# Optimization experiments

Measured on AMD Instinct MI355X. Metric: run time of the kernel, lower is better.

The kernel has to match this reference:

```python
import jax, jax.numpy as jnp
import numpy as np
import math

EPS = 1e-5

def _bn_lrelu(x, g, b, m, v):
    # BatchNorm2d (eval, running stats) + LeakyReLU(0.01)
    inv = jax.lax.rsqrt(v + EPS)
    xn = (x - m[None, :, None, None]) * (g * inv)[None, :, None, None] + b[None, :, None, None]
    return jnp.where(xn >= 0, xn, 0.01 * xn)

def _conv3x3(x, w, b):
    # zero pad 1 on freq (dim2) and time (dim3) (pad_left state is None -> zeros), valid 3x3 conv
    x = jnp.pad(x, ((0, 0), (0, 0), (1, 1), (1, 1)))
    y = jax.lax.conv_general_dilated(x, w, (1, 1), 'VALID',
                                     dimension_numbers=('NCHW', 'OIHW', 'NCHW'))
    return y + b[None, :, None, None]

def _conv1x1(x, w, b):
    return jnp.einsum('bcft,oc->boft', x, w[:, :, 0, 0]) + b[None, :, None, None]

def _blockx3(x, g, b, m, v, w, wb):
    return _conv3x3(_bn_lrelu(x, g, b, m, v), w, wb)

def _mha(x, wqkv, bqkv, wo, bo, n_heads=4, L=64, U=128):
    # banded local attention over time, window = (L back, L fwd), chunked by U
    B, C, F, T = x.shape
    H = n_heads; D = C // H; S = 2 * L
    qkv = _conv1x1(x, wqkv, bqkv)                 # [B,3C,F,T]
    qkv = qkv.transpose(0, 2, 1, 3)               # [B,F,3C,T]
    def split(a):
        return a.reshape(B * F, H, D, T).transpose(0, 1, 3, 2)  # [BF,H,T,D]
    q = split(qkv[:, :, :C])
    k = split(qkv[:, :, C:2 * C])
    v = split(qkv[:, :, 2 * C:])
    Tkv = T + L                                   # kv padded left by L (zero state)
    nC = T // U
    pad_to = nC * U + S                           # pad kv right so every chunk window exists
    kp = jnp.pad(k, ((0, 0), (0, 0), (L, pad_to - Tkv), (0, 0)))
    vp = jnp.pad(v, ((0, 0), (0, 0), (L, pad_to - Tkv), (0, 0)))
    idx = (jnp.arange(nC) * U)[:, None] + jnp.arange(U + S)[None, :]   # [nC, U+S]
    kc = kp[:, :, idx, :]                         # [BF,H,nC,U+S,D]
    vc = vp[:, :, idx, :]
    qc = q.reshape(B * F, H, nC, U, D)
    i = jnp.arange(U)[:, None]; j = jnp.arange(U + S)[None, :]
    band = (j >= i) & (j <= i + S)                # row i sees cols i..i+S (width 1+2L)
    valid = (jnp.arange(nC)[:, None] * U + jnp.arange(U + S)[None, :]) < Tkv
    mask = (band[None, :, :] & valid[:, None, :]).astype(x.dtype)      # [nC,U,U+S]
    scores = jnp.einsum('bhcqd,bhckd->bhcqk', qc, kc) / math.sqrt(D)
    scores = scores * mask - 10000.0 * (1.0 - mask)
    p = jax.nn.softmax(scores, axis=-1)
    o = jnp.einsum('bhcqk,bhckd->bhcqd', p, vc)   # [BF,H,nC,U,D]
    o = o.reshape(B * F, H, T, D).transpose(0, 1, 3, 2).reshape(B, F, C, T).transpose(0, 2, 1, 3)
    return _conv1x1(o, wo, bo)

def setup_inputs() -> dict:
    key = jax.random.key(0)
    ks = jax.random.split(key, 40)
    d = {}
    d['x'] = jax.random.normal(ks[0], (4, 64, 64, 512), dtype=jnp.float32)
    def bn(i, c, pre):
        d[pre + '_g'] = jax.random.normal(ks[i], (c,), jnp.float32) * 0.1 + 1.0
        d[pre + '_b'] = jax.random.normal(ks[i + 1], (c,), jnp.float32) * 0.1
        d[pre + '_m'] = jax.random.normal(ks[i + 2], (c,), jnp.float32) * 0.1
        d[pre + '_v'] = jax.random.uniform(ks[i + 3], (c,), jnp.float32, 0.5, 1.5)
    def conv(i, o, c, kh, kw, pre):
        fan = c * kh * kw
        d[pre + '_w'] = jax.random.normal(ks[i], (o, c, kh, kw), jnp.float32) / math.sqrt(fan)
        d[pre + '_wb'] = jax.random.normal(ks[i + 1], (o,), jnp.float32) * 0.01
    bn(1, 64, 'bd0');  conv(5, 32, 64, 3, 3, 'bd0')
    bn(7, 96, 'bd1');  conv(11, 32, 96, 3, 3, 'bd1')
    bn(13, 128, 'bdo'); conv(17, 64, 128, 3, 3, 'bdo')
    d['qkv_w'] = jax.random.normal(ks[19], (192, 64, 1, 1), jnp.float32) / math.sqrt(64)
    d['qkv_b'] = jax.random.normal(ks[20], (192,), jnp.float32) * 0.01
    d['o_w'] = jax.random.normal(ks[21], (64, 64, 1, 1), jnp.float32) / math.sqrt(64)
    d['o_b'] = jax.random.normal(ks[22], (64,), jnp.float32) * 0.01
    bn(23, 128, 'sao'); conv(27, 64, 128, 1, 1, 'sao')
    return d

def reference(x,
              bd0_g, bd0_b, bd0_m, bd0_v, bd0_w, bd0_wb,
              bd1_g, bd1_b, bd1_m, bd1_v, bd1_w, bd1_wb,
              bdo_g, bdo_b, bdo_m, bdo_v, bdo_w, bdo_wb,
              qkv_w, qkv_b, o_w, o_b,
              sao_g, sao_b, sao_m, sao_v, sao_w, sao_wb):
    # dense conv stack: 64 -> +32 -> +32 -> 64
    a0 = _blockx3(x, bd0_g, bd0_b, bd0_m, bd0_v, bd0_w, bd0_wb)
    x1 = jnp.concatenate([x, a0], axis=1)                 # [B,96,F,T]
    a1 = _blockx3(x1, bd1_g, bd1_b, bd1_m, bd1_v, bd1_w, bd1_wb)
    x2 = jnp.concatenate([x1, a1], axis=1)                # [B,128,F,T]
    y = _blockx3(x2, bdo_g, bdo_b, bdo_m, bdo_v, bdo_w, bdo_wb)  # [B,64,F,T]
    # banded self-attention branch
    att = _mha(y, qkv_w, qkv_b, o_w, o_b)                 # [B,64,F,T]
    z = jnp.concatenate([y, att], axis=1)                 # [B,128,F,T]
    out = _conv1x1(_bn_lrelu(z, sao_g, sao_b, sao_m, sao_v), sao_w, sao_wb)
    return out
```

## Files before the change

### kernel.cpp

```cpp
#include <hip/hip_runtime.h>
#include <hip/hip_bf16.h>

typedef unsigned short u16t;
typedef __attribute__((ext_vector_type(8))) short bfrag;
typedef __attribute__((ext_vector_type(4))) float f32x4;
typedef __attribute__((ext_vector_type(8))) unsigned short uh8;

__device__ __forceinline__ float bfu(u16t u) {
    union { unsigned int i; float f; } c;
    c.i = ((unsigned int)u) << 16;
    return c.f;
}
__device__ __forceinline__ u16t fbf(float f) {
    __hip_bfloat16 h = __float2bfloat16(f);
    return *reinterpret_cast<u16t*>(&h);
}

__global__ __launch_bounds__(256) void prep_x_k(
    const float* __restrict__ x, u16t* __restrict__ xt)
{
    constexpr int F = 64, T = 512;
    __shared__ u16t su[64][74];
    const int tid = threadIdx.x;
    const int t0 = blockIdx.x * 64;
    const int f = blockIdx.y, b = blockIdx.z;

#pragma unroll
    for (int p = 0; p < 16; p++) {
        int i = tid + 256 * p;
        int c = i >> 6, t = i & 63;
        su[c][t] = fbf(x[(((long)b * 64 + c) * F + f) * T + t0 + t]);
    }
    __syncthreads();
#pragma unroll
    for (int p = 0; p < 2; p++) {
        int i = tid + 256 * p;
        int t = i >> 3, c8 = i & 7;
        uh8 v;
#pragma unroll
        for (int j = 0; j < 8; j++) v[j] = su[c8 * 8 + j][t];
        *(uh8*)&xt[(((long)b * F + f) * T + t0 + t) * 64 + c8 * 8] = v;
    }
}

__global__ __launch_bounds__(256) void prep_w_k(
    const float* __restrict__ w0, const float* __restrict__ w1,
    const float* __restrict__ w2, const float* __restrict__ ow,
    const float* __restrict__ sw, const float* __restrict__ qw,
    u16t* __restrict__ wp)
{
    int idx = blockIdx.x * 256 + threadIdx.x;
    if (idx >= 144384) return;
    if (idx < 119808) {
        int C_IN, C_OUT, e;
        const float* src;
        if (idx < 18432)      { C_IN = 64;  C_OUT = 32; src = w0; e = idx; }
        else if (idx < 46080) { C_IN = 96;  C_OUT = 32; src = w1; e = idx - 18432; }
        else                  { C_IN = 128; C_OUT = 64; src = w2; e = idx - 46080; }
        int NCOT = C_OUT / 16;
        int j  = e & 7;
        int l  = (e >> 3) & 63;
        int r  = e >> 9;
        int ct = r % NCOT;
        int r2 = r / NCOT;
        int kk = r2 % 9;
        int cb = r2 / 9;
        int co  = ct * 16 + (l & 15);
        int kin = cb * 32 + (l >> 4) * 8 + j;
        int kh = kk / 3, kw = kk % 3;
        wp[idx] = fbf(src[((co * C_IN + kin) * 3 + kh) * 3 + kw]);
    } else if (idx < 123904) {
        int e = idx - 119808;
        int ks = e & 31, co = (e >> 5) & 63, kb = e >> 11;
        wp[idx] = fbf(ow[co * 64 + kb * 32 + ks]);
    } else if (idx < 132096) {
        int e = idx - 123904;
        int ks = e & 31, co = (e >> 5) & 63, kb = e >> 11;
        wp[idx] = fbf(sw[co * 128 + kb * 32 + ks]);
    } else {
        int e = idx - 132096;
        int ks = e & 31, co = (e >> 5) % 192, kb = e / 6144;
        wp[idx] = fbf(qw[co * 64 + kb * 32 + ks]);
    }
}

template<int C_IN, int C_OUT, bool OBF>
__global__ __launch_bounds__(256) void conv3x3_mfma_k(
    const u16t* __restrict__ s0, const u16t* __restrict__ s1,
    const u16t* __restrict__ s2,
    const float* __restrict__ gg, const float* __restrict__ bb,
    const float* __restrict__ mm, const float* __restrict__ vv,
    const u16t* __restrict__ wseg, const float* __restrict__ wb,
    void* __restrict__ dstv)
{
    constexpr int F = 64, T = 512, TT = 64;
    constexpr int NCH  = C_IN / 32;
    constexpr int NCOT = C_OUT / 16;
    constexpr int WT   = 9 * NCOT * 64;

    __shared__ __align__(16) u16t s_x[3][66][40];
    __shared__ __align__(16) u16t s_w[WT * 8];
    __shared__ float s_scA[C_IN], s_shA[C_IN];

    const int tid = threadIdx.x;
    const int t0 = blockIdx.x * TT;
    const int f  = blockIdx.y;
    const int b  = blockIdx.z;

    if (tid < C_IN) {
        float s = gg[tid] * rsqrtf(vv[tid] + 1e-5f);
        s_scA[tid] = s;
        s_shA[tid] = bb[tid] - mm[tid] * s;
    }

    const int l  = tid & 63;
    const int wv = tid >> 6;
    const int lr = l & 15;
    const int lq = l >> 4;
    const int tbase = wv * 16 + lr;

    f32x4 acc[NCOT];
#pragma unroll
    for (int i = 0; i < NCOT; i++) acc[i] = (f32x4){0.f, 0.f, 0.f, 0.f};

    for (int ch = 0; ch < NCH; ch++) {
        __syncthreads();

        for (int idx = tid; idx < 792 + WT; idx += 256) {
            if (idx < 792) {
                int row = idx >> 2, oct = idx & 3;
                int kh = (row >= 132) ? 2 : ((row >= 66) ? 1 : 0);
                int tp = row - kh * 66;
                int fi = f + kh - 1;
                int tg = t0 + tp - 1;
                int gc8 = ch * 4 + oct;
                uh8 v = (uh8)0;
                if ((unsigned)fi < (unsigned)F && (unsigned)tg < (unsigned)T) {
                    const u16t* sp; int coff, cw;
                    if (gc8 < 8)       { sp = s0; coff = gc8 * 8;        cw = 64; }
                    else if (gc8 < 12) { sp = s1; coff = (gc8 - 8) * 8;  cw = 32; }
                    else               { sp = s2; coff = (gc8 - 12) * 8; cw = 32; }
                    uh8 raw = *(const uh8*)&sp[(((long)b * F + fi) * T + tg) * cw + coff];
#pragma unroll
                    for (int j = 0; j < 8; j++) {
                        float xv = bfu(raw[j]);
                        float xn = fmaf(xv, s_scA[gc8 * 8 + j], s_shA[gc8 * 8 + j]);
                        v[j] = fbf(fmaxf(xn, 0.01f * xn));
                    }
                }
                *(uh8*)&s_x[kh][tp][oct * 8] = v;
            } else {
                int w = idx - 792;
                *(uh8*)&s_w[w * 8] = *(const uh8*)&wseg[((long)ch * WT + w) * 8];
            }
        }
        __syncthreads();

#pragma unroll
        for (int kk = 0; kk < 9; kk++) {
            const int kh = kk / 3, kw = kk % 3;
            bfrag B = *(const bfrag*)&s_x[kh][tbase + kw][lq * 8];
#pragma unroll
            for (int ct = 0; ct < NCOT; ct++) {
                bfrag A = *(const bfrag*)&s_w[((kk * NCOT + ct) * 64 + l) * 8];
                acc[ct] = __builtin_amdgcn_mfma_f32_16x16x32_bf16(A, B, acc[ct], 0, 0, 0);
            }
        }
    }

    const int t = t0 + wv * 16 + lr;
#pragma unroll
    for (int ct = 0; ct < NCOT; ct++) {
        int co0 = ct * 16 + lq * 4;
        float4 bs = *(const float4*)&wb[co0];
        long obase = (((long)b * F + f) * T + t) * C_OUT + co0;
        if (OBF) {
            u16t* dp = (u16t*)dstv;
            ushort4 pk;
            pk.x = fbf(acc[ct][0] + bs.x);
            pk.y = fbf(acc[ct][1] + bs.y);
            pk.z = fbf(acc[ct][2] + bs.z);
            pk.w = fbf(acc[ct][3] + bs.w);
            *(ushort4*)&dp[obase] = pk;
        } else {
            float* dp = (float*)dstv;
            float4 ov;
            ov.x = acc[ct][0] + bs.x;
            ov.y = acc[ct][1] + bs.y;
            ov.z = acc[ct][2] + bs.z;
            ov.w = acc[ct][3] + bs.w;
            *(float4*)&dp[obase] = ov;
        }
    }
}

__global__ __launch_bounds__(256) void qkv_mfma_k(
    const u16t* __restrict__ ybf, const u16t* __restrict__ wq,
    const float* __restrict__ qbias,
    u16t* __restrict__ q_t, u16t* __restrict__ k_t, u16t* __restrict__ v_t)
{
    constexpr int F = 64, T = 512;
    __shared__ __align__(16) u16t s_y[64][72];
    const int tid = threadIdx.x;
    const int t0 = blockIdx.x * 64;
    const int f = blockIdx.y, b = blockIdx.z;
    const long bf = (long)b * F + f;

    for (int i = tid; i < 512; i += 256) {
        int tt = i >> 3, c0 = (i & 7) * 8;
        *(uh8*)&s_y[tt][c0] = *(const uh8*)&ybf[(bf * T + t0 + tt) * 64 + c0];
    }
    __syncthreads();

    const int l = tid & 63, wv = tid >> 6;
    const int lr = l & 15, lq = l >> 4;
    const int tb = wv * 16 + lr;

    bfrag B0 = *(const bfrag*)&s_y[tb][lq * 8];
    bfrag B1 = *(const bfrag*)&s_y[tb][32 + lq * 8];

    f32x4 acc[12];
#pragma unroll
    for (int i = 0; i < 12; i++) acc[i] = (f32x4){0.f, 0.f, 0.f, 0.f};
#pragma unroll
    for (int ct = 0; ct < 12; ct++) {
        bfrag A0 = *(const bfrag*)&wq[(ct * 16 + lr) * 32 + lq * 8];
        acc[ct] = __builtin_amdgcn_mfma_f32_16x16x32_bf16(A0, B0, acc[ct], 0, 0, 0);
    }
#pragma unroll
    for (int ct = 0; ct < 12; ct++) {
        bfrag A1 = *(const bfrag*)&wq[(192 + ct * 16 + lr) * 32 + lq * 8];
        acc[ct] = __builtin_amdgcn_mfma_f32_16x16x32_bf16(A1, B1, acc[ct], 0, 0, 0);
    }

    const int t = t0 + tb;
#pragma unroll
    for (int ct = 0; ct < 12; ct++) {
        int co0 = ct * 16 + lq * 4;
        float4 bi = *(const float4*)&qbias[co0];
        float a0 = acc[ct][0] + bi.x, a1 = acc[ct][1] + bi.y;
        float a2 = acc[ct][2] + bi.z, a3 = acc[ct][3] + bi.w;
        if (co0 < 64) {
            ushort4 pk;
            pk.x = fbf(a0 * 0.25f); pk.y = fbf(a1 * 0.25f);
            pk.z = fbf(a2 * 0.25f); pk.w = fbf(a3 * 0.25f);
            *(ushort4*)&q_t[(bf * T + t) * 64 + co0] = pk;
        } else if (co0 < 128) {
            int hh = (co0 - 64) >> 4, d0 = (co0 - 64) & 15;
            ushort4 pk;
            pk.x = fbf(a0); pk.y = fbf(a1); pk.z = fbf(a2); pk.w = fbf(a3);
            *(ushort4*)&k_t[((bf * 4 + hh) * T + t) * 16 + d0] = pk;
        } else {
            int hh = (co0 - 128) >> 4, d0 = (co0 - 128) & 15;
            long vb = (bf * 4 + hh) * 16;
            v_t[(vb + d0 + 0) * T + t] = fbf(a0);
            v_t[(vb + d0 + 1) * T + t] = fbf(a1);
            v_t[(vb + d0 + 2) * T + t] = fbf(a2);
            v_t[(vb + d0 + 3) * T + t] = fbf(a3);
        }
    }
}

__global__ __launch_bounds__(256) void attn_mfma_k(
    const u16t* __restrict__ qt, const u16t* __restrict__ kt_,
    const u16t* __restrict__ vt, u16t* __restrict__ ob)
{
    constexpr int T = 512, F = 64;
    const int qc = blockIdx.x & 7;
    const int h  = blockIdx.x >> 3;
    const int f = blockIdx.y, b = blockIdx.z;
    const int qb0 = qc * 64;
    const int tid = threadIdx.x;
    const long bf = (long)b * F + f;
    const long kvb = bf * 4 + h;

    __shared__ __align__(16) u16t s_k[192][24];
    __shared__ __align__(16) u16t s_v[16][216];
    __shared__ __align__(16) u16t s_p[4][16][168];
    __shared__ __align__(16) u16t s_zero[8];

    if (tid < 8) s_zero[tid] = 0;

    for (int idx = tid; idx < 384; idx += 256) {
        int kk = idx >> 1, hv = idx & 1;
        int p = qb0 - 64 + kk;
        uh8 v = (uh8)0;
        if ((unsigned)p < (unsigned)T)
            v = *(const uh8*)&kt_[(kvb * T + p) * 16 + hv * 8];
        *(uh8*)&s_k[kk][hv * 8] = v;
    }
    for (int idx = tid; idx < 432; idx += 256) {
        int d = idx / 27, c8 = idx % 27;
        int kk0 = c8 * 8;
        int p0 = qb0 - 64 + kk0;
        uh8 v = (uh8)0;
        if (p0 >= 0 && p0 + 7 < T) {
            v = *(const uh8*)&vt[(kvb * 16 + d) * T + p0];
        } else {
#pragma unroll
            for (int j = 0; j < 8; j++) {
                int p = p0 + j;
                v[j] = ((unsigned)p < (unsigned)T)
                     ? vt[(kvb * 16 + d) * T + p] : (u16t)0;
            }
        }
        *(uh8*)&s_v[d][kk0] = v;
    }
    __syncthreads();

    const int l  = tid & 63;
    const int wv = tid >> 6;
    const int lr = l & 15;
    const int lq = l >> 4;
    const int qt0 = qb0 + wv * 16;

    bfrag Bq = (bfrag)0;
    if (lq < 2)
        Bq = *(const bfrag*)&qt[(bf * T + qt0 + lr) * 64 + h * 16 + lq * 8];

    f32x4 sf[9];
#pragma unroll
    for (int kti = 0; kti < 9; kti++) {
        const u16t* ap = (lq < 2) ? &s_k[wv * 16 + kti * 16 + lr][lq * 8]
                                  : &s_zero[0];
        bfrag A = *(const bfrag*)ap;
        sf[kti] = __builtin_amdgcn_mfma_f32_16x16x32_bf16(
            A, Bq, (f32x4){0.f, 0.f, 0.f, 0.f}, 0, 0, 0);
    }

    float m = -3.0e38f;
#pragma unroll
    for (int kti = 0; kti < 9; kti++) {
#pragma unroll
        for (int j = 0; j < 4; j++) {
            int rk = kti * 16 + lq * 4 + j;
            int dq = rk - lr;
            int p  = qt0 - 64 + rk;
            float s = sf[kti][j];
            s = (dq >= 0 && dq <= 128 && p < T) ? s : -1.0e30f;
            sf[kti][j] = s;
            m = fmaxf(m, s);
        }
    }
    m = fmaxf(m, __shfl_xor(m, 16));
    m = fmaxf(m, __shfl_xor(m, 32));

    float lsum = 0.f;
#pragma unroll
    for (int kti = 0; kti < 9; kti++) {
#pragma unroll
        for (int j = 0; j < 4; j++) {
            float e = __expf(sf[kti][j] - m);
            sf[kti][j] = e;
            lsum += e;
        }
    }
    lsum += __shfl_xor(lsum, 16);
    lsum += __shfl_xor(lsum, 32);

#pragma unroll
    for (int kti = 0; kti < 9; kti++) {
        ushort4 pk;
        pk.x = fbf(sf[kti][0]); pk.y = fbf(sf[kti][1]);
        pk.z = fbf(sf[kti][2]); pk.w = fbf(sf[kti][3]);
        *(ushort4*)&s_p[wv][lr][kti * 16 + lq * 4] = pk;
    }
    {
        ushort4 z; z.x = 0; z.y = 0; z.z = 0; z.w = 0;
        *(ushort4*)&s_p[wv][lr][144 + lq * 4] = z;
    }
    __syncthreads();

    f32x4 oa = (f32x4){0.f, 0.f, 0.f, 0.f};
#pragma unroll
    for (int kc = 0; kc < 5; kc++) {
        bfrag Av = *(const bfrag*)&s_v[lr][wv * 16 + kc * 32 + lq * 8];
        bfrag Bp = *(const bfrag*)&s_p[wv][lr][kc * 32 + lq * 8];
        oa = __builtin_amdgcn_mfma_f32_16x16x32_bf16(Av, Bp, oa, 0, 0, 0);
    }
    const float inv = 1.0f / lsum;
    ushort4 ov;
    ov.x = fbf(oa[0] * inv); ov.y = fbf(oa[1] * inv);
    ov.z = fbf(oa[2] * inv); ov.w = fbf(oa[3] * inv);
    *(ushort4*)&ob[(bf * T + qt0 + lr) * 64 + h * 16 + lq * 4] = ov;
}

__global__ __launch_bounds__(256) void final_mfma_k(
    const u16t* __restrict__ ob, const u16t* __restrict__ yb,
    const u16t* __restrict__ wo, const float* __restrict__ obias,
    const float* __restrict__ sg, const float* __restrict__ sb,
    const float* __restrict__ sm, const float* __restrict__ sv,
    const u16t* __restrict__ wsao, const float* __restrict__ swb,
    float* __restrict__ out)
{
    constexpr int F = 64, T = 512, TT = 64, P = 72;
    __shared__ __align__(16) u16t s_ob[64][P];
    __shared__ __align__(16) u16t s_y2[64][P];
    __shared__ __align__(16) u16t s_att[64][P];
    __shared__ float s_sc[128], s_sh[128];

    const int tid = threadIdx.x;
    const int t0 = blockIdx.x * TT;
    const int f = blockIdx.y, b = blockIdx.z;

    if (tid < 128) {
        float sc = sg[tid] * rsqrtf(sv[tid] + 1e-5f);
        s_sc[tid] = sc;
        s_sh[tid] = sb[tid] - sm[tid] * sc;
    }
    __syncthreads();

    for (int i = tid; i < 512; i += 256) {
        int tt = i >> 3, c0 = (i & 7) * 8;
        long gi = (((long)b * F + f) * T + t0 + tt) * 64 + c0;
        *(uh8*)&s_ob[tt][c0] = *(const uh8*)&ob[gi];
        uh8 raw = *(const uh8*)&yb[gi];
        uh8 v;
#pragma unroll
        for (int j = 0; j < 8; j++) {
            float xv = bfu(raw[j]);
            float xn = fmaf(xv, s_sc[c0 + j], s_sh[c0 + j]);
            v[j] = fbf(fmaxf(xn, 0.01f * xn));
        }
        *(uh8*)&s_y2[tt][c0] = v;
    }
    __syncthreads();

    const int l  = tid & 63;
    const int wv = tid >> 6;
    const int lr = l & 15;
    const int lq = l >> 4;
    const int tbase = wv * 16 + lr;
    const int cbase = lq * 8;

    f32x4 acc1[4];
#pragma unroll
    for (int i = 0; i < 4; i++) acc1[i] = (f32x4){0.f, 0.f, 0.f, 0.f};
#pragma unroll
    for (int kb = 0; kb < 2; kb++) {
        bfrag B = *(const bfrag*)&s_ob[tbase][kb * 32 + cbase];
#pragma unroll
        for (int ct = 0; ct < 4; ct++) {
            bfrag A = *(const bfrag*)&wo[(kb * 64 + ct * 16 + lr) * 32 + lq * 8];
            acc1[ct] = __builtin_amdgcn_mfma_f32_16x16x32_bf16(A, B, acc1[ct], 0, 0, 0);
        }
    }
#pragma unroll
    for (int ct = 0; ct < 4; ct++) {
        int co = ct * 16 + lq * 4;
        float4 bi = *(const float4*)&obias[co];
#pragma unroll
        for (int j = 0; j < 4; j++) {
            float a = acc1[ct][j] + ((j == 0) ? bi.x : (j == 1) ? bi.y : (j == 2) ? bi.z : bi.w);
            int cg = 64 + co + j;
            float xn = fmaf(a, s_sc[cg], s_sh[cg]);
            s_att[tbase][co + j] = fbf(fmaxf(xn, 0.01f * xn));
        }
    }
    __syncthreads();

    f32x4 acc2[4];
#pragma unroll
    for (int i = 0; i < 4; i++) acc2[i] = (f32x4){0.f, 0.f, 0.f, 0.f};
#pragma unroll
    for (int kb = 0; kb < 4; kb++) {
        bfrag B = (kb < 2) ? *(const bfrag*)&s_y2[tbase][kb * 32 + cbase]
                           : *(const bfrag*)&s_att[tbase][(kb - 2) * 32 + cbase];
#pragma unroll
        for (int ct = 0; ct < 4; ct++) {
            bfrag A = *(const bfrag*)&wsao[(kb * 64 + ct * 16 + lr) * 32 + lq * 8];
            acc2[ct] = __builtin_amdgcn_mfma_f32_16x16x32_bf16(A, B, acc2[ct], 0, 0, 0);
        }
    }
    const int t = t0 + wv * 16 + lr;
#pragma unroll
    for (int ct = 0; ct < 4; ct++) {
        int co0 = ct * 16 + lq * 4;
        float4 bs = *(const float4*)&swb[co0];
#pragma unroll
        for (int j = 0; j < 4; j++) {
            float bv = (j == 0) ? bs.x : (j == 1) ? bs.y : (j == 2) ? bs.z : bs.w;
            out[(((long)b * 64 + co0 + j) * F + f) * T + t] = acc2[ct][j] + bv;
        }
    }
}

extern "C" void kernel_launch(void* const* d_in, const int* in_sizes, int n_in,
                              void* d_out, int out_size, void* d_ws, size_t ws_size,
                              hipStream_t stream)
{
    (void)in_sizes; (void)n_in; (void)out_size; (void)ws_size;

    const float* x      = (const float*)d_in[0];
    const float* bd0_g  = (const float*)d_in[1];
    const float* bd0_b  = (const float*)d_in[2];
    const float* bd0_m  = (const float*)d_in[3];
    const float* bd0_v  = (const float*)d_in[4];
    const float* bd0_w  = (const float*)d_in[5];
    const float* bd0_wb = (const float*)d_in[6];
    const float* bd1_g  = (const float*)d_in[7];
    const float* bd1_b  = (const float*)d_in[8];
    const float* bd1_m  = (const float*)d_in[9];
    const float* bd1_v  = (const float*)d_in[10];
    const float* bd1_w  = (const float*)d_in[11];
    const float* bd1_wb = (const float*)d_in[12];
    const float* bdo_g  = (const float*)d_in[13];
    const float* bdo_b  = (const float*)d_in[14];
    const float* bdo_m  = (const float*)d_in[15];
    const float* bdo_v  = (const float*)d_in[16];
    const float* bdo_w  = (const float*)d_in[17];
    const float* bdo_wb = (const float*)d_in[18];
    const float* qkv_w  = (const float*)d_in[19];
    const float* qkv_b  = (const float*)d_in[20];
    const float* o_w    = (const float*)d_in[21];
    const float* o_b    = (const float*)d_in[22];
    const float* sao_g  = (const float*)d_in[23];
    const float* sao_b  = (const float*)d_in[24];
    const float* sao_m  = (const float*)d_in[25];
    const float* sao_v  = (const float*)d_in[26];
    const float* sao_w  = (const float*)d_in[27];
    const float* sao_wb = (const float*)d_in[28];

    char* ws = (char*)d_ws;
    u16t* xt  = (u16t*)(ws);
    u16t* a0  = (u16t*)(ws + 16777216);
    u16t* a1  = (u16t*)(ws + 25165824);
    u16t* q_t = (u16t*)(ws);
    u16t* k_t = (u16t*)(ws + 16777216);
    u16t* v_t = (u16t*)(ws + 33554432);
    u16t* ybf = (u16t*)(ws + 50331648);
    u16t* obf = q_t;
    u16t* wpk = (u16t*)(ws + 67108864);

    dim3 blk(256);
    dim3 gconv(8, 64, 4);

    hipLaunchKernelGGL(prep_x_k, gconv, blk, 0, stream, x, xt);
    hipLaunchKernelGGL(prep_w_k, dim3(564), blk, 0, stream,
        bd0_w, bd1_w, bdo_w, o_w, sao_w, qkv_w, wpk);
    hipLaunchKernelGGL((conv3x3_mfma_k<64, 32, true>), gconv, blk, 0, stream,
        xt, nullptr, nullptr, bd0_g, bd0_b, bd0_m, bd0_v, wpk, bd0_wb, (void*)a0);
    hipLaunchKernelGGL((conv3x3_mfma_k<96, 32, true>), gconv, blk, 0, stream,
        xt, a0, nullptr, bd1_g, bd1_b, bd1_m, bd1_v, wpk + 18432, bd1_wb, (void*)a1);
    hipLaunchKernelGGL((conv3x3_mfma_k<128, 64, true>), gconv, blk, 0, stream,
        xt, a0, a1, bdo_g, bdo_b, bdo_m, bdo_v, wpk + 46080, bdo_wb, (void*)ybf);
    hipLaunchKernelGGL(qkv_mfma_k, gconv, blk, 0, stream,
        ybf, wpk + 132096, qkv_b, q_t, k_t, v_t);
    hipLaunchKernelGGL(attn_mfma_k, dim3(32, 64, 4), blk, 0, stream,
        q_t, k_t, v_t, obf);
    hipLaunchKernelGGL(final_mfma_k, gconv, blk, 0, stream,
        obf, ybf, wpk + 119808, o_b, sao_g, sao_b, sao_m, sao_v,
        wpk + 123904, sao_wb, (float*)d_out);
}
```

Baseline: 211.2 us.

## Precompute BN-activated inputs in producers and tile conv over four frequency rows

Conv3x3 blocks now compute four frequency rows per block (one per wave), staging six input rows in LDS and reusing each weight fragment across four time subtiles. This cuts weight reloads and halo re-reads. BatchNorm+LeakyReLU is no longer applied while staging conv inputs. Instead, the prep kernel and conv epilogues write pre-normalised bf16 copies tailored to each downstream conv, which adds extra global writes and workspace.

```diff
diff --git a/kernel.cpp b/kernel.cpp
--- a/kernel.cpp
+++ b/kernel.cpp
@@ -16,15 +16,30 @@
     return *reinterpret_cast<u16t*>(&h);
 }
 
-__global__ __launch_bounds__(256) void prep_x_k(
-    const float* __restrict__ x, u16t* __restrict__ xt)
+__global__ __launch_bounds__(256) void prep_x3_k(
+    const float* __restrict__ x,
+    const float* __restrict__ g0, const float* __restrict__ b0,
+    const float* __restrict__ m0, const float* __restrict__ v0,
+    const float* __restrict__ g1, const float* __restrict__ b1,
+    const float* __restrict__ m1, const float* __restrict__ v1,
+    const float* __restrict__ g2, const float* __restrict__ b2,
+    const float* __restrict__ m2, const float* __restrict__ v2,
+    u16t* __restrict__ xn0, u16t* __restrict__ xn1, u16t* __restrict__ xn2)
 {
     constexpr int F = 64, T = 512;
     __shared__ u16t su[64][74];
+    __shared__ float ssc[3][64], ssh[3][64];
     const int tid = threadIdx.x;
     const int t0 = blockIdx.x * 64;
     const int f = blockIdx.y, b = blockIdx.z;
 
+    if (tid < 64) {
+        int c = tid;
+        float s;
+        s = g0[c] * rsqrtf(v0[c] + 1e-5f); ssc[0][c] = s; ssh[0][c] = b0[c] - m0[c] * s;
+        s = g1[c] * rsqrtf(v1[c] + 1e-5f); ssc[1][c] = s; ssh[1][c] = b1[c] - m1[c] * s;
+        s = g2[c] * rsqrtf(v2[c] + 1e-5f); ssc[2][c] = s; ssh[2][c] = b2[c] - m2[c] * s;
+    }
 #pragma unroll
     for (int p = 0; p < 16; p++) {
         int i = tid + 256 * p;
@@ -36,10 +51,22 @@
     for (int p = 0; p < 2; p++) {
         int i = tid + 256 * p;
         int t = i >> 3, c8 = i & 7;
-        uh8 v;
-#pragma unroll
-        for (int j = 0; j < 8; j++) v[j] = su[c8 * 8 + j][t];
-        *(uh8*)&xt[(((long)b * F + f) * T + t0 + t) * 64 + c8 * 8] = v;
+        uh8 o0, o1, o2;
+#pragma unroll
+        for (int j = 0; j < 8; j++) {
+            int c = c8 * 8 + j;
+            float xv = bfu(su[c][t]);
+            float n0 = fmaf(xv, ssc[0][c], ssh[0][c]);
+            float n1 = fmaf(xv, ssc[1][c], ssh[1][c]);
+            float n2 = fmaf(xv, ssc[2][c], ssh[2][c]);
+            o0[j] = fbf(fmaxf(n0, 0.01f * n0));
+            o1[j] = fbf(fmaxf(n1, 0.01f * n1));
+            o2[j] = fbf(fmaxf(n2, 0.01f * n2));
+        }
+        long gi = (((long)b * F + f) * T + t0 + t) * 64 + c8 * 8;
+        *(uh8*)&xn0[gi] = o0;
+        *(uh8*)&xn1[gi] = o1;
+        *(uh8*)&xn2[gi] = o2;
     }
 }
 
@@ -84,73 +111,65 @@
     }
 }
 
-template<int C_IN, int C_OUT, bool OBF>
-__global__ __launch_bounds__(256) void conv3x3_mfma_k(
+template<int C_IN, int C_OUT, int EPI>
+__global__ __launch_bounds__(256) void conv3x3_ff4_k(
     const u16t* __restrict__ s0, const u16t* __restrict__ s1,
     const u16t* __restrict__ s2,
-    const float* __restrict__ gg, const float* __restrict__ bb,
-    const float* __restrict__ mm, const float* __restrict__ vv,
     const u16t* __restrict__ wseg, const float* __restrict__ wb,
-    void* __restrict__ dstv)
+    const float* __restrict__ g1, const float* __restrict__ b1,
+    const float* __restrict__ m1, const float* __restrict__ v1,
+    const float* __restrict__ g2, const float* __restrict__ b2,
+    const float* __restrict__ m2, const float* __restrict__ v2,
+    int bnoff, u16t* __restrict__ dst1, u16t* __restrict__ dst2)
 {
-    constexpr int F = 64, T = 512, TT = 64;
+    constexpr int F = 64, T = 512, TT = 64, FF = 4;
     constexpr int NCH  = C_IN / 32;
     constexpr int NCOT = C_OUT / 16;
-    constexpr int WT   = 9 * NCOT * 64;
-
-    __shared__ __align__(16) u16t s_x[3][66][40];
+    constexpr int WT = 9 * NCOT * 64;
+    constexpr int XT = 6 * 66 * 4;
+
+    __shared__ __align__(16) u16t s_x[6][66][40];
     __shared__ __align__(16) u16t s_w[WT * 8];
-    __shared__ float s_scA[C_IN], s_shA[C_IN];
 
     const int tid = threadIdx.x;
     const int t0 = blockIdx.x * TT;
-    const int f  = blockIdx.y;
+    const int f0 = blockIdx.y * FF;
     const int b  = blockIdx.z;
-
-    if (tid < C_IN) {
-        float s = gg[tid] * rsqrtf(vv[tid] + 1e-5f);
-        s_scA[tid] = s;
-        s_shA[tid] = bb[tid] - mm[tid] * s;
-    }
 
     const int l  = tid & 63;
     const int wv = tid >> 6;
     const int lr = l & 15;
     const int lq = l >> 4;
-    const int tbase = wv * 16 + lr;
-
-    f32x4 acc[NCOT];
-#pragma unroll
-    for (int i = 0; i < NCOT; i++) acc[i] = (f32x4){0.f, 0.f, 0.f, 0.f};
+
+    f32x4 acc[4][NCOT];
+#pragma unroll
+    for (int i = 0; i < 4; i++)
+#pragma unroll
+        for (int j = 0; j < NCOT; j++) acc[i][j] = (f32x4){0.f, 0.f, 0.f, 0.f};
 
     for (int ch = 0; ch < NCH; ch++) {
-        __syncthreads();
-
-        for (int idx = tid; idx < 792 + WT; idx += 256) {
-            if (idx < 792) {
-                int row = idx >> 2, oct = idx & 3;
-                int kh = (row >= 132) ? 2 : ((row >= 66) ? 1 : 0);
-                int tp = row - kh * 66;
-                int fi = f + kh - 1;
+        if (ch) __syncthreads();
+
+        for (int idx = tid; idx < XT + WT; idx += 256) {
+            if (idx < XT) {
+                int oct = idx & 3;
+                int row = idx >> 2;
+                int fr = row / 66;
+                int tp = row - fr * 66;
+                int fi = f0 + fr - 1;
                 int tg = t0 + tp - 1;
                 int gc8 = ch * 4 + oct;
                 uh8 v = (uh8)0;
                 if ((unsigned)fi < (unsigned)F && (unsigned)tg < (unsigned)T) {
                     const u16t* sp; int coff, cw;
-                    if (gc8 < 8)       { sp = s0; coff = gc8 * 8;        cw = 64; }
-                    else if (gc8 < 12) { sp = s1; coff = (gc8 - 8) * 8;  cw = 32; }
-                    else               { sp = s2; coff = (gc8 - 12) * 8; cw = 32; }
-                    uh8 raw = *(const uh8*)&sp[(((long)b * F + fi) * T + tg) * cw + coff];
-#pragma unroll
-                    for (int j = 0; j < 8; j++) {
-                        float xv = bfu(raw[j]);
-                        float xn = fmaf(xv, s_scA[gc8 * 8 + j], s_shA[gc8 * 8 + j]);
-                        v[j] = fbf(fmaxf(xn, 0.01f * xn));
-                    }
+                    if (C_IN == 64 || gc8 < 8) { sp = s0; coff = gc8 * 8;        cw = 64; }
+                    else if (gc8 < 12)         { sp = s1; coff = (gc8 - 8) * 8;  cw = 32; }
+                    else                       { sp = s2; coff = (gc8 - 12) * 8; cw = 32; }
+                    v = *(const uh8*)&sp[(((long)b * F + fi) * T + tg) * cw + coff];
                 }
-                *(uh8*)&s_x[kh][tp][oct * 8] = v;
+                *(uh8*)&s_x[fr][tp][oct * 8] = v;
             } else {
-                int w = idx - 792;
+                int w = idx - XT;
                 *(uh8*)&s_w[w * 8] = *(const uh8*)&wseg[((long)ch * WT + w) * 8];
             }
         }
@@ -159,37 +178,75 @@
 #pragma unroll
         for (int kk = 0; kk < 9; kk++) {
             const int kh = kk / 3, kw = kk % 3;
-            bfrag B = *(const bfrag*)&s_x[kh][tbase + kw][lq * 8];
-#pragma unroll
-            for (int ct = 0; ct < NCOT; ct++) {
-                bfrag A = *(const bfrag*)&s_w[((kk * NCOT + ct) * 64 + l) * 8];
-                acc[ct] = __builtin_amdgcn_mfma_f32_16x16x32_bf16(A, B, acc[ct], 0, 0, 0);
+            bfrag A[NCOT];
+#pragma unroll
+            for (int ct = 0; ct < NCOT; ct++)
+                A[ct] = *(const bfrag*)&s_w[((kk * NCOT + ct) * 64 + l) * 8];
+#pragma unroll
+            for (int ts = 0; ts < 4; ts++) {
+                bfrag B = *(const bfrag*)&s_x[wv + kh][ts * 16 + lr + kw][lq * 8];
+#pragma unroll
+                for (int ct = 0; ct < NCOT; ct++)
+                    acc[ts][ct] = __builtin_amdgcn_mfma_f32_16x16x32_bf16(
+                        A[ct], B, acc[ts][ct], 0, 0, 0);
             }
         }
     }
 
-    const int t = t0 + wv * 16 + lr;
+    const int f = f0 + wv;
 #pragma unroll
     for (int ct = 0; ct < NCOT; ct++) {
-        int co0 = ct * 16 + lq * 4;
+        const int co0 = ct * 16 + lq * 4;
         float4 bs = *(const float4*)&wb[co0];
-        long obase = (((long)b * F + f) * T + t) * C_OUT + co0;
-        if (OBF) {
-            u16t* dp = (u16t*)dstv;
-            ushort4 pk;
-            pk.x = fbf(acc[ct][0] + bs.x);
-            pk.y = fbf(acc[ct][1] + bs.y);
-            pk.z = fbf(acc[ct][2] + bs.z);
-            pk.w = fbf(acc[ct][3] + bs.w);
-            *(ushort4*)&dp[obase] = pk;
-        } else {
-            float* dp = (float*)dstv;
-            float4 ov;
-            ov.x = acc[ct][0] + bs.x;
-            ov.y = acc[ct][1] + bs.y;
-            ov.z = acc[ct][2] + bs.z;
-            ov.w = acc[ct][3] + bs.w;
-            *(float4*)&dp[obase] = ov;
+        float sc1[4], sh1[4], sc2[4], sh2[4];
+        if (EPI >= 1) {
+#pragma unroll
+            for (int j = 0; j < 4; j++) {
+                int c = bnoff + co0 + j;
+                float s = g1[c] * rsqrtf(v1[c] + 1e-5f);
+                sc1[j] = s; sh1[j] = b1[c] - m1[c] * s;
+            }
+        }
+        if (EPI == 2) {
+#pragma unroll
+            for (int j = 0; j < 4; j++) {
+                int c = bnoff + co0 + j;
+                float s = g2[c] * rsqrtf(v2[c] + 1e-5f);
+                sc2[j] = s; sh2[j] = b2[c] - m2[c] * s;
+            }
+        }
+#pragma unroll
+        for (int ts = 0; ts < 4; ts++) {
+            const int t = t0 + ts * 16 + lr;
+            long ob = (((long)b * F + f) * T + t) * C_OUT + co0;
+            float a[4];
+            a[0] = acc[ts][ct][0] + bs.x;
+            a[1] = acc[ts][ct][1] + bs.y;
+            a[2] = acc[ts][ct][2] + bs.z;
+            a[3] = acc[ts][ct][3] + bs.w;
+            if (EPI == 0) {
+                ushort4 pk;
+                pk.x = fbf(a[0]); pk.y = fbf(a[1]);
+                pk.z = fbf(a[2]); pk.w = fbf(a[3]);
+                *(ushort4*)&dst1[ob] = pk;
+            } else {
+                ushort4 p1;
+#pragma unroll
+                for (int j = 0; j < 4; j++) {
+                    float n = fmaf(a[j], sc1[j], sh1[j]);
+                    ((u16t*)&p1)[j] = fbf(fmaxf(n, 0.01f * n));
+                }
+                *(ushort4*)&dst1[ob] = p1;
+                if (EPI == 2) {
+                    ushort4 p2;
+#pragma unroll
+                    for (int j = 0; j < 4; j++) {
+                        float n = fmaf(a[j], sc2[j], sh2[j]);
+                        ((u16t*)&p2)[j] = fbf(fmaxf(n, 0.01f * n));
+                    }
+                    *(ushort4*)&dst2[ob] = p2;
+                }
+            }
         }
     }
 }
@@ -522,33 +579,45 @@
     const float* sao_wb = (const float*)d_in[28];
 
     char* ws = (char*)d_ws;
-    u16t* xt  = (u16t*)(ws);
-    u16t* a0  = (u16t*)(ws + 16777216);
-    u16t* a1  = (u16t*)(ws + 25165824);
-    u16t* q_t = (u16t*)(ws);
-    u16t* k_t = (u16t*)(ws + 16777216);
-    u16t* v_t = (u16t*)(ws + 33554432);
-    u16t* ybf = (u16t*)(ws + 50331648);
-    u16t* obf = q_t;
-    u16t* wpk = (u16t*)(ws + 67108864);
+    u16t* xn0  = (u16t*)(ws);
+    u16t* xn1  = (u16t*)(ws + 16777216);
+    u16t* xn2  = (u16t*)(ws + 33554432);
+    u16t* a0n1 = (u16t*)(ws + 50331648);
+    u16t* a0n2 = (u16t*)(ws + 58720256);
+    u16t* a1n2 = (u16t*)(ws + 67108864);
+    u16t* ybf  = xn0;
+    u16t* q_t  = xn1;
+    u16t* k_t  = xn2;
+    u16t* v_t  = a0n1;
+    u16t* obf  = q_t;
+    u16t* wpk  = (u16t*)(ws + 75497472);
 
     dim3 blk(256);
-    dim3 gconv(8, 64, 4);
-
-    hipLaunchKernelGGL(prep_x_k, gconv, blk, 0, stream, x, xt);
+    dim3 gprep(8, 64, 4);
+    dim3 gconv(8, 16, 4);
+
+    hipLaunchKernelGGL(prep_x3_k, gprep, blk, 0, stream, x,
+        bd0_g, bd0_b, bd0_m, bd0_v, bd1_g, bd1_b, bd1_m, bd1_v,
+        bdo_g, bdo_b, bdo_m, bdo_v, xn0, xn1, xn2);
     hipLaunchKernelGGL(prep_w_k, dim3(564), blk, 0, stream,
         bd0_w, bd1_w, bdo_w, o_w, sao_w, qkv_w, wpk);
-    hipLaunchKernelGGL((conv3x3_mfma_k<64, 32, true>), gconv, blk, 0, stream,
-        xt, nullptr, nullptr, bd0_g, bd0_b, bd0_m, bd0_v, wpk, bd0_wb, (void*)a0);
-    hipLaunchKernelGGL((conv3x3_mfma_k<96, 32, true>), gconv, blk, 0, stream,
-        xt, a0, nullptr, bd1_g, bd1_b, bd1_m, bd1_v, wpk + 18432, bd1_wb, (void*)a1);
-    hipLaunchKernelGGL((conv3x3_mfma_k<128, 64, true>), gconv, blk, 0, stream,
-        xt, a0, a1, bdo_g, bdo_b, bdo_m, bdo_v, wpk + 46080, bdo_wb, (void*)ybf);
-    hipLaunchKernelGGL(qkv_mfma_k, gconv, blk, 0, stream,
+    hipLaunchKernelGGL((conv3x3_ff4_k<64, 32, 2>), gconv, blk, 0, stream,
+        xn0, nullptr, nullptr, wpk, bd0_wb,
+        bd1_g, bd1_b, bd1_m, bd1_v, bdo_g, bdo_b, bdo_m, bdo_v,
+        64, a0n1, a0n2);
+    hipLaunchKernelGGL((conv3x3_ff4_k<96, 32, 1>), gconv, blk, 0, stream,
+        xn1, a0n1, nullptr, wpk + 18432, bd1_wb,
+        bdo_g, bdo_b, bdo_m, bdo_v, nullptr, nullptr, nullptr, nullptr,
+        96, a1n2, nullptr);
+    hipLaunchKernelGGL((conv3x3_ff4_k<128, 64, 0>), gconv, blk, 0, stream,
+        xn2, a0n2, a1n2, wpk + 46080, bdo_wb,
+        nullptr, nullptr, nullptr, nullptr, nullptr, nullptr, nullptr, nullptr,
+        0, ybf, nullptr);
+    hipLaunchKernelGGL(qkv_mfma_k, gprep, blk, 0, stream,
         ybf, wpk + 132096, qkv_b, q_t, k_t, v_t);
     hipLaunchKernelGGL(attn_mfma_k, dim3(32, 64, 4), blk, 0, stream,
         q_t, k_t, v_t, obf);
-    hipLaunchKernelGGL(final_mfma_k, gconv, blk, 0, stream,
+    hipLaunchKernelGGL(final_mfma_k, gprep, blk, 0, stream,
         obf, ybf, wpk + 119808, o_b, sao_g, sao_b, sao_m, sao_v,
         wpk + 123904, sao_wb, (float*)d_out);
 }
```

Result: faster. 182.4 us (-13.6%).
